# Kernel optimization log

Measured on AMD Instinct MI355X. Metric: run time of the kernel, lower is better.

The kernel has to match this reference:

```python
import jax, jax.numpy as jnp
import numpy as np

B, U, W = 64, 128, 128  # batch, input_units, window_size (output units == U)

def setup_inputs() -> dict:
    key = jax.random.key(0)
    k1, k2, k3 = jax.random.split(key, 3)
    return {
        "input_tensor": jax.random.normal(k1, (B, U), dtype=jnp.float32),
        "state": jax.random.normal(k2, (B, U, W), dtype=jnp.float32),
        "w": jax.random.normal(k3, (2 * U + 1, U), dtype=jnp.float32) * 0.05,
        "b": jnp.zeros((U,), dtype=jnp.float32),
    }

def reference(input_tensor, state, w, b):
    b_, u_, w_ = state.shape
    # state @ state_shift is exactly a left-shift along the window axis
    new_state = jnp.concatenate([state[:, :, 1:], input_tensor[:, :, None]], axis=-1)  # [B,U,W]
    # NOTE: original uses tf.reshape (NOT transpose) [B,U,W] -> [B,W,U]; we replicate that
    flip = new_state.reshape(b_, w_, u_)                      # [B,W,U]
    # h_i[b,i,j,:] = flip[b,j,:] (stacked on axis=1); h_j[b,i,j,:] = flip[b,i,:]
    dot = jnp.einsum('biu,bju->bij', flip, flip)              # h_i . h_j, [B,W,W]
    w_hi, w_hj, w_dot = w[:u_], w[u_:2 * u_], w[2 * u_]       # split concat-matmul
    sim = (jnp.einsum('bju,uv->bjv', flip, w_hi)[:, None, :, :]   # h_i part
           + jnp.einsum('biu,uv->biv', flip, w_hj)[:, :, None, :] # h_j part
           + dot[..., None] * w_dot + b)                          # [B,W,W,U]
    a = jax.nn.softmax(sim, axis=2)                           # softmax over axis=-2 (j)
    c = jnp.einsum('bju,biju->biu', flip, a)                  # sum_j h_i * a_ij
    return c[:, -1, :]                                        # c_last, [B,U]
```

## Files before the change

### kernel.cpp

```cpp
#include <hip/hip_runtime.h>
#include <hip/hip_bf16.h>

constexpr int Bx = 64, Ux = 128, Wx = 128;
constexpr int NS = 4;
constexpr int VC = 32;
constexpr int LDST = 136;
constexpr int LDWT = 136;
constexpr int LDA  = 129;

typedef __attribute__((ext_vector_type(8))) short s16x8;
typedef __attribute__((ext_vector_type(4))) float fx4;

static __device__ __forceinline__ short f2b(float x) {
  union { float f; unsigned u; } c; c.f = x;
  unsigned r = c.u + 0x7fffu + ((c.u >> 16) & 1u);
  return (short)(r >> 16);
}
static __device__ __forceinline__ float b2f(short s) {
  union { unsigned u; float f; } c; c.u = ((unsigned)(unsigned short)s) << 16;
  return c.f;
}

__global__ __launch_bounds__(256) void rsa_kernel(const float* __restrict__ input,
                                                  const float* __restrict__ state,
                                                  const float* __restrict__ w,
                                                  float* __restrict__ out) {
  __shared__ __align__(16) short st_s[Wx][LDST];
  __shared__ __align__(16) short wst[VC][LDWT];
  __shared__ float a_s[VC][LDA];
  __shared__ float red_s[8][VC];
  __shared__ float wdot_s[VC], w127_s[VC];
  __shared__ float dpart[4];

  const int t = threadIdx.x;
  const int s = blockIdx.x, b = blockIdx.y;
  const int vb = s * VC;
  const float* stb = state + (size_t)b * Ux * Wx;
  const float* inb = input + (size_t)b * Ux;

#pragma unroll
  for (int i = 0; i < 4; ++i) {
    int g = i * 4096 + t * 16;
    int j = g >> 7, k = g & 127;
    const float4* src = reinterpret_cast<const float4*>(stb + g);
    float4 x0 = src[0], x1 = src[1], x2 = src[2], x3 = src[3];
    s16x8 p0 = { f2b(x0.x), f2b(x0.y), f2b(x0.z), f2b(x0.w),
                 f2b(x1.x), f2b(x1.y), f2b(x1.z), f2b(x1.w) };
    s16x8 p1 = { f2b(x2.x), f2b(x2.y), f2b(x2.z), f2b(x2.w),
                 f2b(x3.x), f2b(x3.y), f2b(x3.z), f2b(x3.w) };
    *reinterpret_cast<s16x8*>(&st_s[j][k])     = p0;
    *reinterpret_cast<s16x8*>(&st_s[j][k + 8]) = p1;
  }
  if (t < Wx) st_s[t][128] = f2b(inb[t]);
  for (int idx = t; idx < 127 * VC; idx += 256) {
    int r = idx >> 5, v = idx & (VC - 1);
    wst[v][r + 1] = f2b(w[r * Ux + vb + v]);
  }
  if (t < VC) { wst[t][0] = 0; w127_s[t] = w[127 * Ux + vb + t]; }
  else if (t < 2 * VC) { wdot_s[t - VC] = w[2 * Ux * Ux + vb + (t - VC)]; }
  {
    float part = 0.f;
    if (t < Wx) { float x = (t < Wx - 1) ? stb[127 * Wx + t + 1] : inb[127]; part = x * x; }
#pragma unroll
    for (int off = 32; off; off >>= 1) part += __shfl_down(part, off);
    if ((t & 63) == 0) dpart[t >> 6] = part;
  }
  __syncthreads();

  const int wv = t >> 6, l = t & 63, lc = l & 15, lg = l >> 4;
  fx4 accH[2][2] = {};
  fx4 accD[2]    = {};
#pragma unroll
  for (int kt = 0; kt < 4; ++kt) {
    const int ko = kt * 32 + lg * 8;
    s16x8 bd = *reinterpret_cast<const s16x8*>(&st_s[127][ko]);
    s16x8 b0 = *reinterpret_cast<const s16x8*>(&wst[lc][ko]);
    s16x8 b1 = *reinterpret_cast<const s16x8*>(&wst[lc + 16][ko]);
#pragma unroll
    for (int jl = 0; jl < 2; ++jl) {
      const int jt = wv * 2 + jl;
      s16x8 a = *reinterpret_cast<const s16x8*>(&st_s[jt * 16 + lc][ko]);
      accH[jl][0] = __builtin_amdgcn_mfma_f32_16x16x32_bf16(a, b0, accH[jl][0], 0, 0, 0);
      accH[jl][1] = __builtin_amdgcn_mfma_f32_16x16x32_bf16(a, b1, accH[jl][1], 0, 0, 0);
      accD[jl]    = __builtin_amdgcn_mfma_f32_16x16x32_bf16(a, bd, accD[jl],    0, 0, 0);
    }
  }

  const float in127  = b2f(st_s[127][128]);
  const float st0127 = b2f(st_s[127][0]);
  const float d127   = dpart[0] + dpart[1] + dpart[2] + dpart[3];
  const float wd0 = wdot_s[lc], wd1 = wdot_s[lc + 16];
  const float w70 = w127_s[lc], w71 = w127_s[lc + 16];
#pragma unroll
  for (int jl = 0; jl < 2; ++jl) {
    const int jt = wv * 2 + jl;
#pragma unroll
    for (int r = 0; r < 4; ++r) {
      const int row = jt * 16 + lg * 4 + r;
      float st0 = b2f(st_s[row][0]);
      float inr = b2f(st_s[row][128]);
      float dotv = accD[jl][r] - st0 * st0127 + inr * in127;
      if (row == Wx - 1) dotv = d127;
      a_s[lc][row]      = accH[jl][0][r] + dotv * wd0 + inr * w70;
      a_s[lc + 16][row] = accH[jl][1][r] + dotv * wd1 + inr * w71;
    }
  }
  __syncthreads();

  const int v = t & 31, sub = t >> 5;
  const int jb = sub * 16;
  float m = -3.4e38f;
#pragma unroll
  for (int k = 0; k < 16; ++k) m = fmaxf(m, a_s[v][jb + k]);
  red_s[sub][v] = m;
  __syncthreads();
  float M = red_s[0][v];
#pragma unroll
  for (int r = 1; r < 8; ++r) M = fmaxf(M, red_s[r][v]);
  __syncthreads();
  float ssum = 0.f;
#pragma unroll
  for (int k = 0; k < 16; ++k) {
    float e = __expf(a_s[v][jb + k] - M);
    a_s[v][jb + k] = e;
    ssum += e;
  }
  red_s[sub][v] = ssum;
  __syncthreads();
  float S = 0.f;
#pragma unroll
  for (int r = 0; r < 8; ++r) S += red_s[r][v];
  __syncthreads();

  float p = 0.f;
#pragma unroll
  for (int k = 0; k < 16; ++k) {
    int j = jb + k;
    p = fmaf(b2f(st_s[j][vb + v + 1]), a_s[v][j], p);
  }
  red_s[sub][v] = p;
  __syncthreads();
  if (sub == 0) {
    float o = 0.f;
#pragma unroll
    for (int r = 0; r < 8; ++r) o += red_s[r][v];
    out[(size_t)b * Ux + vb + v] = o / S;
  }
}

extern "C" void kernel_launch(void* const* d_in, const int* in_sizes, int n_in,
                              void* d_out, int out_size, void* d_ws, size_t ws_size,
                              hipStream_t stream) {
  const float* input = (const float*)d_in[0];
  const float* state = (const float*)d_in[1];
  const float* w     = (const float*)d_in[2];
  float* out = (float*)d_out;
  dim3 grid(NS, Bx);
  rsa_kernel<<<grid, dim3(256), 0, stream>>>(input, state, w, out);
}
```

Before: 66.85 us.

## Merge column-split blocks into one 1024-thread block per batch with register softmax

Replaces the 4-block-per-batch split over output columns with a single 1024-thread block per batch that loads the state tile once and computes all 128 output columns. The 4x redundant state loading and bf16 conversion disappear. The softmax and weighted sum are now done from MFMA accumulator registers using wave shuffles and small cross-wave reductions, replacing the LDS score matrix and its many barrier phases. In exchange the grid shrinks from 256 to 64 blocks, so fewer CUs are busy. The transposed weight store also uses strided scalar LDS writes.

Result: no change. 67.97 us (+1.7%).

```diff
diff --git a/kernel.cpp b/kernel.cpp
--- a/kernel.cpp
+++ b/kernel.cpp
@@ -2,13 +2,11 @@
 #include <hip/hip_bf16.h>
 
 constexpr int Bx = 64, Ux = 128, Wx = 128;
-constexpr int NS = 4;
-constexpr int VC = 32;
 constexpr int LDST = 136;
 constexpr int LDWT = 136;
-constexpr int LDA  = 129;
 
 typedef __attribute__((ext_vector_type(8))) short s16x8;
+typedef __attribute__((ext_vector_type(4))) short s16x4;
 typedef __attribute__((ext_vector_type(4))) float fx4;
 
 static __device__ __forceinline__ short f2b(float x) {
@@ -21,130 +19,138 @@
   return c.f;
 }
 
-__global__ __launch_bounds__(256) void rsa_kernel(const float* __restrict__ input,
-                                                  const float* __restrict__ state,
-                                                  const float* __restrict__ w,
-                                                  float* __restrict__ out) {
+__global__ __launch_bounds__(1024) void rsa_kernel(const float* __restrict__ input,
+                                                   const float* __restrict__ state,
+                                                   const float* __restrict__ w,
+                                                   float* __restrict__ out) {
   __shared__ __align__(16) short st_s[Wx][LDST];
-  __shared__ __align__(16) short wst[VC][LDWT];
-  __shared__ float a_s[VC][LDA];
-  __shared__ float red_s[8][VC];
-  __shared__ float wdot_s[VC], w127_s[VC];
-  __shared__ float dpart[4];
+  __shared__ __align__(16) short wst[Wx][LDWT];
+  __shared__ float colmax[4][128], colsum[4][128], ppart[4][128];
+  __shared__ float w127_s[128], wdot_s[128];
+  __shared__ float dpart[2];
 
   const int t = threadIdx.x;
-  const int s = blockIdx.x, b = blockIdx.y;
-  const int vb = s * VC;
+  const int b = blockIdx.x;
   const float* stb = state + (size_t)b * Ux * Wx;
   const float* inb = input + (size_t)b * Ux;
 
 #pragma unroll
   for (int i = 0; i < 4; ++i) {
-    int g = i * 4096 + t * 16;
-    int j = g >> 7, k = g & 127;
-    const float4* src = reinterpret_cast<const float4*>(stb + g);
-    float4 x0 = src[0], x1 = src[1], x2 = src[2], x3 = src[3];
-    s16x8 p0 = { f2b(x0.x), f2b(x0.y), f2b(x0.z), f2b(x0.w),
-                 f2b(x1.x), f2b(x1.y), f2b(x1.z), f2b(x1.w) };
-    s16x8 p1 = { f2b(x2.x), f2b(x2.y), f2b(x2.z), f2b(x2.w),
-                 f2b(x3.x), f2b(x3.y), f2b(x3.z), f2b(x3.w) };
-    *reinterpret_cast<s16x8*>(&st_s[j][k])     = p0;
-    *reinterpret_cast<s16x8*>(&st_s[j][k + 8]) = p1;
+    int F = i * 1024 + t;
+    int j = F >> 5, k4 = (F & 31) * 4;
+    float4 x = *reinterpret_cast<const float4*>(stb + (size_t)F * 4);
+    s16x4 p = { f2b(x.x), f2b(x.y), f2b(x.z), f2b(x.w) };
+    *reinterpret_cast<s16x4*>(&st_s[j][k4]) = p;
   }
   if (t < Wx) st_s[t][128] = f2b(inb[t]);
-  for (int idx = t; idx < 127 * VC; idx += 256) {
-    int r = idx >> 5, v = idx & (VC - 1);
-    wst[v][r + 1] = f2b(w[r * Ux + vb + v]);
+#pragma unroll
+  for (int i = 0; i < 4; ++i) {
+    int F = i * 1024 + t;
+    if (F < 4064) {
+      int r = F >> 5, v4 = (F & 31) * 4;
+      float4 x = *reinterpret_cast<const float4*>(w + r * Ux + v4);
+      wst[v4 + 0][r + 1] = f2b(x.x);
+      wst[v4 + 1][r + 1] = f2b(x.y);
+      wst[v4 + 2][r + 1] = f2b(x.z);
+      wst[v4 + 3][r + 1] = f2b(x.w);
+    }
   }
-  if (t < VC) { wst[t][0] = 0; w127_s[t] = w[127 * Ux + vb + t]; }
-  else if (t < 2 * VC) { wdot_s[t - VC] = w[2 * Ux * Ux + vb + (t - VC)]; }
-  {
-    float part = 0.f;
-    if (t < Wx) { float x = (t < Wx - 1) ? stb[127 * Wx + t + 1] : inb[127]; part = x * x; }
+  if (t < Wx) { wst[t][0] = 0; w127_s[t] = w[127 * Ux + t]; }
+  else if (t < 2 * Wx) wdot_s[t - Wx] = w[2 * Ux * Ux + (t - Wx)];
+  if (t < Wx) {
+    float x = (t < Wx - 1) ? stb[127 * Wx + t + 1] : inb[127];
+    float p = x * x;
 #pragma unroll
-    for (int off = 32; off; off >>= 1) part += __shfl_down(part, off);
-    if ((t & 63) == 0) dpart[t >> 6] = part;
+    for (int off = 32; off; off >>= 1) p += __shfl_down(p, off);
+    if ((t & 63) == 0) dpart[t >> 6] = p;
   }
   __syncthreads();
 
   const int wv = t >> 6, l = t & 63, lc = l & 15, lg = l >> 4;
-  fx4 accH[2][2] = {};
-  fx4 accD[2]    = {};
+  const int wr = wv >> 2, wc = wv & 3;
+  fx4 aH[2][2] = {};
+  fx4 aD[2] = {};
 #pragma unroll
   for (int kt = 0; kt < 4; ++kt) {
     const int ko = kt * 32 + lg * 8;
     s16x8 bd = *reinterpret_cast<const s16x8*>(&st_s[127][ko]);
-    s16x8 b0 = *reinterpret_cast<const s16x8*>(&wst[lc][ko]);
-    s16x8 b1 = *reinterpret_cast<const s16x8*>(&wst[lc + 16][ko]);
+    s16x8 b0 = *reinterpret_cast<const s16x8*>(&wst[wc * 32 + lc][ko]);
+    s16x8 b1 = *reinterpret_cast<const s16x8*>(&wst[wc * 32 + 16 + lc][ko]);
 #pragma unroll
     for (int jl = 0; jl < 2; ++jl) {
-      const int jt = wv * 2 + jl;
-      s16x8 a = *reinterpret_cast<const s16x8*>(&st_s[jt * 16 + lc][ko]);
-      accH[jl][0] = __builtin_amdgcn_mfma_f32_16x16x32_bf16(a, b0, accH[jl][0], 0, 0, 0);
-      accH[jl][1] = __builtin_amdgcn_mfma_f32_16x16x32_bf16(a, b1, accH[jl][1], 0, 0, 0);
-      accD[jl]    = __builtin_amdgcn_mfma_f32_16x16x32_bf16(a, bd, accD[jl],    0, 0, 0);
+      s16x8 a = *reinterpret_cast<const s16x8*>(&st_s[wr * 32 + jl * 16 + lc][ko]);
+      aH[jl][0] = __builtin_amdgcn_mfma_f32_16x16x32_bf16(a, b0, aH[jl][0], 0, 0, 0);
+      aH[jl][1] = __builtin_amdgcn_mfma_f32_16x16x32_bf16(a, b1, aH[jl][1], 0, 0, 0);
+      aD[jl]    = __builtin_amdgcn_mfma_f32_16x16x32_bf16(a, bd, aD[jl],    0, 0, 0);
     }
   }
 
   const float in127  = b2f(st_s[127][128]);
   const float st0127 = b2f(st_s[127][0]);
-  const float d127   = dpart[0] + dpart[1] + dpart[2] + dpart[3];
-  const float wd0 = wdot_s[lc], wd1 = wdot_s[lc + 16];
-  const float w70 = w127_s[lc], w71 = w127_s[lc + 16];
+  const float d127   = dpart[0] + dpart[1];
+  const float wd0 = wdot_s[wc * 32 + lc],      wd1 = wdot_s[wc * 32 + 16 + lc];
+  const float w70 = w127_s[wc * 32 + lc],      w71 = w127_s[wc * 32 + 16 + lc];
+  float sim[2][2][4];
 #pragma unroll
   for (int jl = 0; jl < 2; ++jl) {
-    const int jt = wv * 2 + jl;
 #pragma unroll
     for (int r = 0; r < 4; ++r) {
-      const int row = jt * 16 + lg * 4 + r;
+      const int row = wr * 32 + jl * 16 + lg * 4 + r;
       float st0 = b2f(st_s[row][0]);
       float inr = b2f(st_s[row][128]);
-      float dotv = accD[jl][r] - st0 * st0127 + inr * in127;
+      float dotv = aD[jl][r] - st0 * st0127 + inr * in127;
       if (row == Wx - 1) dotv = d127;
-      a_s[lc][row]      = accH[jl][0][r] + dotv * wd0 + inr * w70;
-      a_s[lc + 16][row] = accH[jl][1][r] + dotv * wd1 + inr * w71;
+      sim[jl][0][r] = aH[jl][0][r] + dotv * wd0 + inr * w70;
+      sim[jl][1][r] = aH[jl][1][r] + dotv * wd1 + inr * w71;
     }
+  }
+
+  float m0 = -3.4e38f, m1 = -3.4e38f;
+#pragma unroll
+  for (int jl = 0; jl < 2; ++jl)
+#pragma unroll
+    for (int r = 0; r < 4; ++r) {
+      m0 = fmaxf(m0, sim[jl][0][r]);
+      m1 = fmaxf(m1, sim[jl][1][r]);
+    }
+  m0 = fmaxf(m0, __shfl_xor(m0, 16)); m0 = fmaxf(m0, __shfl_xor(m0, 32));
+  m1 = fmaxf(m1, __shfl_xor(m1, 16)); m1 = fmaxf(m1, __shfl_xor(m1, 32));
+  if (l < 16) { colmax[wr][wc * 32 + l] = m0; colmax[wr][wc * 32 + 16 + l] = m1; }
+  __syncthreads();
+  const float M0 = fmaxf(fmaxf(colmax[0][wc * 32 + lc], colmax[1][wc * 32 + lc]),
+                         fmaxf(colmax[2][wc * 32 + lc], colmax[3][wc * 32 + lc]));
+  const float M1 = fmaxf(fmaxf(colmax[0][wc * 32 + 16 + lc], colmax[1][wc * 32 + 16 + lc]),
+                         fmaxf(colmax[2][wc * 32 + 16 + lc], colmax[3][wc * 32 + 16 + lc]));
+  float s0 = 0.f, s1 = 0.f, p0 = 0.f, p1 = 0.f;
+#pragma unroll
+  for (int jl = 0; jl < 2; ++jl)
+#pragma unroll
+    for (int r = 0; r < 4; ++r) {
+      const int row = wr * 32 + jl * 16 + lg * 4 + r;
+      float e0 = __expf(sim[jl][0][r] - M0);
+      float e1 = __expf(sim[jl][1][r] - M1);
+      s0 += e0; s1 += e1;
+      p0 = fmaf(b2f(st_s[row][wc * 32 + lc + 1]), e0, p0);
+      p1 = fmaf(b2f(st_s[row][wc * 32 + 16 + lc + 1]), e1, p1);
+    }
+  s0 += __shfl_xor(s0, 16); s0 += __shfl_xor(s0, 32);
+  s1 += __shfl_xor(s1, 16); s1 += __shfl_xor(s1, 32);
+  p0 += __shfl_xor(p0, 16); p0 += __shfl_xor(p0, 32);
+  p1 += __shfl_xor(p1, 16); p1 += __shfl_xor(p1, 32);
+  if (l < 16) {
+    colsum[wr][wc * 32 + l] = s0; colsum[wr][wc * 32 + 16 + l] = s1;
+    ppart[wr][wc * 32 + l]  = p0; ppart[wr][wc * 32 + 16 + l]  = p1;
   }
   __syncthreads();
 
-  const int v = t & 31, sub = t >> 5;
-  const int jb = sub * 16;
-  float m = -3.4e38f;
+  if (wr == 0 && l < 16) {
 #pragma unroll
-  for (int k = 0; k < 16; ++k) m = fmaxf(m, a_s[v][jb + k]);
-  red_s[sub][v] = m;
-  __syncthreads();
-  float M = red_s[0][v];
-#pragma unroll
-  for (int r = 1; r < 8; ++r) M = fmaxf(M, red_s[r][v]);
-  __syncthreads();
-  float ssum = 0.f;
-#pragma unroll
-  for (int k = 0; k < 16; ++k) {
-    float e = __expf(a_s[v][jb + k] - M);
-    a_s[v][jb + k] = e;
-    ssum += e;
-  }
-  red_s[sub][v] = ssum;
-  __syncthreads();
-  float S = 0.f;
-#pragma unroll
-  for (int r = 0; r < 8; ++r) S += red_s[r][v];
-  __syncthreads();
-
-  float p = 0.f;
-#pragma unroll
-  for (int k = 0; k < 16; ++k) {
-    int j = jb + k;
-    p = fmaf(b2f(st_s[j][vb + v + 1]), a_s[v][j], p);
-  }
-  red_s[sub][v] = p;
-  __syncthreads();
-  if (sub == 0) {
-    float o = 0.f;
-#pragma unroll
-    for (int r = 0; r < 8; ++r) o += red_s[r][v];
-    out[(size_t)b * Ux + vb + v] = o / S;
+    for (int vl = 0; vl < 2; ++vl) {
+      const int gv = wc * 32 + vl * 16 + l;
+      float S = colsum[0][gv] + colsum[1][gv] + colsum[2][gv] + colsum[3][gv];
+      float P = ppart[0][gv] + ppart[1][gv] + ppart[2][gv] + ppart[3][gv];
+      out[(size_t)b * Ux + gv] = P / S;
+    }
   }
 }
 
@@ -155,6 +161,5 @@
   const float* state = (const float*)d_in[1];
   const float* w     = (const float*)d_in[2];
   float* out = (float*)d_out;
-  dim3 grid(NS, Bx);
-  rsa_kernel<<<grid, dim3(256), 0, stream>>>(input, state, w, out);
+  rsa_kernel<<<dim3(Bx), dim3(1024), 0, stream>>>(input, state, w, out);
 }
```
